# Optimization experiments

Hardware: AMD Instinct MI355X
Metric: run time of the kernel (lower is better)

## Reference

```python
import jax, jax.numpy as jnp
import numpy as np

B, N, C, NH = 32, 1024, 768, 12
KS = 3
KK = KS * KS
HD = C // NH
SCALE = HD ** -0.5
PMD = 2 * C   # patch_mix_dims = int(2 * dim)
CMD = 2 * C   # channel_mix_dims = int(2 * dim)


def _ln(x, g, b, eps):
    m = jnp.mean(x, axis=-1, keepdims=True)
    v = jnp.var(x, axis=-1, keepdims=True)
    return (x - m) * jax.lax.rsqrt(v + eps) * g + b


def setup_inputs() -> dict:
    key = jax.random.key(0)
    ks = jax.random.split(key, 12)
    w = lambda k, shape: jax.random.normal(k, shape, jnp.float32) * 0.02
    return dict(
        x=jax.random.normal(ks[0], (B, N, C), jnp.float32),
        H=32, W=32,
        kernel=w(ks[1], (KK, C)),                 # nn.Parameter, std 0.02
        ln_g=jnp.ones((C,), jnp.float32), ln_b=jnp.zeros((C,), jnp.float32),
        kv_w=w(ks[2], (C, 2 * C)),                # kv Linear, no bias (qkv_bias=False)
        proj_w=w(ks[3], (C, C)), proj_b=jnp.zeros((C,), jnp.float32),
        projq_w=w(ks[4], (C, C)),                 # proj_q, no bias
        n1_g=jnp.ones((C,), jnp.float32), n1_b=jnp.zeros((C,), jnp.float32),
        n2_g=jnp.ones((C,), jnp.float32), n2_b=jnp.zeros((C,), jnp.float32),
        pm1_w=w(ks[5], (KK, PMD)), pm1_b=jnp.zeros((PMD,), jnp.float32),
        pm2_w=w(ks[6], (PMD, KK)), pm2_b=jnp.zeros((KK,), jnp.float32),
        cm1_w=w(ks[7], (C, CMD)), cm1_b=jnp.zeros((CMD,), jnp.float32),
        cm2_w=w(ks[8], (CMD, C)), cm2_b=jnp.zeros((C,), jnp.float32),
    )


def reference(x, H, W, kernel, ln_g, ln_b, kv_w, proj_w, proj_b, projq_w,
              n1_g, n1_b, n2_g, n2_b, pm1_w, pm1_b, pm2_w, pm2_b,
              cm1_w, cm1_b, cm2_w, cm2_b):
    Bv, Nv, Cv = x.shape
    # w: expand learned 3x3 token kernel to batch -> [B, 9, C]
    w0 = jnp.broadcast_to(kernel, (Bv, KK, Cv))
    # queries from LN(kernel): [B, nh, 9, hd]
    wm = _ln(w0, ln_g, ln_b, 1e-6).reshape(Bv, KK, NH, HD).transpose(0, 2, 1, 3)
    # keys/values from x: [B, nh, N, hd]
    kv = (x @ kv_w).reshape(Bv, Nv, 2, NH, HD)
    k = kv[:, :, 0].transpose(0, 2, 1, 3)
    v = kv[:, :, 1].transpose(0, 2, 1, 3)
    attn = jax.nn.softmax(jnp.einsum('bhqd,bhkd->bhqk', wm, k) * SCALE, axis=-1)
    ca = jnp.einsum('bhqk,bhkd->bhqd', attn, v).transpose(0, 2, 1, 3).reshape(Bv, KK, Cv)
    ca = ca @ proj_w + proj_b
    w1 = w0 + ca                                  # [B, 9, C]
    # MLPMixer layer (drop_path = 0 -> identity)
    t = _ln(w1, n1_g, n1_b, 1e-5).transpose(0, 2, 1)              # [B, C, 9]
    t = jax.nn.gelu(t @ pm1_w + pm1_b, approximate=False) @ pm2_w + pm2_b
    w1 = w1 + t.transpose(0, 2, 1)
    t = _ln(w1, n2_g, n2_b, 1e-5)
    w1 = w1 + (jax.nn.gelu(t @ cm1_w + cm1_b, approximate=False) @ cm2_w + cm2_b)
    # dynamic per-(batch,channel) 3x3 depthwise conv
    filt = w1.transpose(0, 2, 1).reshape(Bv * Cv, 1, KS, KS)       # [B*C, 1, 3, 3]
    xq = (x @ projq_w).transpose(0, 2, 1).reshape(1, Bv * Cv, H, W)
    y = jax.lax.conv_general_dilated(
        xq, filt, window_strides=(1, 1), padding=((1, 1), (1, 1)),
        feature_group_count=Bv * Cv,
        dimension_numbers=('NCHW', 'OIHW', 'NCHW'))
    return y.reshape(Bv, Cv, H * W).transpose(0, 2, 1)             # [B, N, C]
```

## Files before the change

kernel.cpp:

```cpp
#include <hip/hip_runtime.h>
#include <hip/hip_bf16.h>
#include <cstdint>
#include <cstddef>

typedef __attribute__((ext_vector_type(8))) short bf16x8;
typedef __attribute__((ext_vector_type(4))) float f32x4;

#define BB 32
#define NN 1024
#define CC 768
#define NHH 12
#define HDD 64
#define KKK 9
#define MM (BB * NN)
#define KN2 1664
#define PMDD 1536
#define CMDD 1536
#define BK 64

#define XBF_BLOCKS 12288
#define WT_BLOCKS 1152
#define WT2_BLOCKS 2880
#define SW_BLOCKS 128

__device__ __forceinline__ float bfbits2f(short s) {
  union { uint32_t u; float f; } cv;
  cv.u = ((uint32_t)(uint16_t)s) << 16;
  return cv.f;
}
__device__ __forceinline__ short f2bf(float f) {
  union { float f; uint32_t u; } cv;
  cv.f = f;
  uint32_t u = cv.u;
  uint32_t r = (u + 0x7fffu + ((u >> 16) & 1u)) >> 16;
  return (short)r;
}
__device__ __forceinline__ float gelu_f(float x) {
  return 0.5f * x * (1.0f + erff(x * 0.7071067811865476f));
}

typedef const __attribute__((address_space(1))) uint32_t* gp1_t;
typedef __attribute__((address_space(3))) uint32_t* lp3_t;
__device__ __forceinline__ void gload16(const short* g, const short* l) {
  __builtin_amdgcn_global_load_lds((gp1_t)(uintptr_t)(const void*)g,
                                   (lp3_t)(uint32_t)(uintptr_t)(const void*)l,
                                   16, 0, 0);
}

__global__ __launch_bounds__(256) void prep_kernel(
    const float* __restrict__ x, short* __restrict__ xb,
    const float* __restrict__ kv_w, const float* __restrict__ projq_w,
    short* __restrict__ Wt,
    const float* __restrict__ proj_w, const float* __restrict__ cm1_w,
    const float* __restrict__ cm2_w,
    short* __restrict__ WpT, short* __restrict__ Wc1T, short* __restrict__ Wc2T,
    const float* __restrict__ kern, const float* __restrict__ ln_g,
    const float* __restrict__ ln_b)
{
  __shared__ float smem[1056];
  const int bx = blockIdx.x;
  const int tid = threadIdx.x;
  if (bx < XBF_BLOCKS) {
    const int i = (bx * 256 + tid) * 8;
    f32x4 a = *(const f32x4*)&x[i];
    f32x4 b = *(const f32x4*)&x[i + 4];
    bf16x8 o;
#pragma unroll
    for (int e = 0; e < 4; e++) { o[e] = f2bf(a[e]); o[e + 4] = f2bf(b[e]); }
    *(bf16x8*)&xb[i] = o;
    return;
  }
  if (bx < XBF_BLOCKS + WT_BLOCKS) {
    int b2 = bx - XBF_BLOCKS;
    int j0 = (b2 % 48) * 32;
    int c0 = (b2 / 48) * 32;
    const float* src; int ldj, jj;
    if (j0 < 768) { src = kv_w; ldj = 1536; jj = 768 + j0; }
    else          { src = projq_w; ldj = 768; jj = j0 - 768; }
    const int tx = tid & 31, ty = tid >> 5;
#pragma unroll
    for (int r = 0; r < 4; r++) {
      int cl = ty + r * 8;
      smem[cl * 33 + tx] = src[(size_t)(c0 + cl) * ldj + jj + tx];
    }
    __syncthreads();
#pragma unroll
    for (int r = 0; r < 4; r++) {
      int jl = ty + r * 8;
      Wt[(size_t)(j0 + jl) * CC + c0 + tx] = f2bf(smem[tx * 33 + jl]);
    }
    return;
  }
  if (bx < XBF_BLOCKS + WT_BLOCKS + WT2_BLOCKS) {
    int b2 = bx - XBF_BLOCKS - WT_BLOCKS;
    const float* src; short* dst; int ldj, ldc, j0, c0;
    if (b2 < 576)        { src = proj_w; dst = WpT;  ldj = 768;  ldc = 768;
                           j0 = (b2 % 24) * 32; c0 = (b2 / 24) * 32; }
    else if (b2 < 1728)  { b2 -= 576; src = cm1_w; dst = Wc1T; ldj = 1536; ldc = 768;
                           j0 = (b2 % 48) * 32; c0 = (b2 / 48) * 32; }
    else                 { b2 -= 1728; src = cm2_w; dst = Wc2T; ldj = 768; ldc = 1536;
                           j0 = (b2 % 24) * 32; c0 = (b2 / 24) * 32; }
    const int tx = tid & 31, ty = tid >> 5;
#pragma unroll
    for (int r = 0; r < 4; r++) {
      int cl = ty + r * 8;
      smem[cl * 33 + tx] = src[(size_t)(c0 + cl) * ldj + j0 + tx];
    }
    __syncthreads();
#pragma unroll
    for (int r = 0; r < 4; r++) {
      int jl = ty + r * 8;
      dst[(size_t)(j0 + jl) * ldc + c0 + tx] = f2bf(smem[tx * 33 + jl]);
    }
    return;
  }
  {
    const int s = bx - (XBF_BLOCKS + WT_BLOCKS + WT2_BLOCKS);
    if (s >= 108) {
      const size_t r = (size_t)(1536 + s) * CC;
      Wt[r + tid] = 0; Wt[r + tid + 256] = 0; Wt[r + tid + 512] = 0;
      return;
    }
    const int h = s / 9, q = s % 9;
    float* red = smem;
    const size_t base = (size_t)q * CC;
    float x0 = kern[base + tid];
    float x1 = kern[base + tid + 256];
    float x2 = kern[base + tid + 512];
    red[tid] = x0 + x1 + x2;
    __syncthreads();
    for (int st = 128; st > 0; st >>= 1) { if (tid < st) red[tid] += red[tid + st]; __syncthreads(); }
    float mean = red[0] * (1.0f / 768.0f);
    __syncthreads();
    float d0 = x0 - mean, d1 = x1 - mean, d2 = x2 - mean;
    red[tid] = d0 * d0 + d1 * d1 + d2 * d2;
    __syncthreads();
    for (int st = 128; st > 0; st >>= 1) { if (tid < st) red[tid] += red[tid + st]; __syncthreads(); }
    float rstd = rsqrtf(red[0] * (1.0f / 768.0f) + 1e-6f);
    __syncthreads();
    smem[tid]       = d0 * rstd * ln_g[tid]       + ln_b[tid];
    smem[tid + 256] = d1 * rstd * ln_g[tid + 256] + ln_b[tid + 256];
    smem[tid + 512] = d2 * rstd * ln_g[tid + 512] + ln_b[tid + 512];
    __syncthreads();
#pragma unroll
    for (int k = 0; k < 3; k++) {
      const int cc = tid + k * 256;
      const float* kw = &kv_w[(size_t)cc * 1536 + h * HDD];
      float acc = 0.f;
#pragma unroll
      for (int dd = 0; dd < HDD; dd++) acc += smem[h * HDD + dd] * kw[dd];
      Wt[(size_t)(1536 + s) * CC + cc] = f2bf(acc * 0.125f);
    }
  }
}

__global__ __launch_bounds__(256) void gemm_bt_kernel(
    const short* __restrict__ A,
    const short* __restrict__ Bt,
    short* __restrict__ C)
{
  __shared__ short As[2][128 * BK];
  __shared__ short Bs[2][128 * BK];
  const int tid = threadIdx.x;
  const int wave = tid >> 6, lane = tid & 63;
  const int lid = blockIdx.x;
  const int wid = (lid & 7) * 416 + (lid >> 3);
  const int bn = (wid % 13) * 128;
  const int bm = (wid / 13) * 128;
  const int wmo = (wave >> 1) * 64;
  const int wno = (wave & 1) * 64;
  const int lrow = lane & 15;
  const int kgrp = lane >> 4;
  const int sr = tid >> 3;
  const int ss = tid & 7;
  const int slotG = ss ^ (sr & 7);
  const short* gA = A + (size_t)(bm + sr) * CC + slotG * 8;
  const short* gB = Bt + (size_t)(bn + sr) * CC + slotG * 8;
  const int rs0 = kgrp ^ (lrow & 7);
  const int rs1 = (4 + kgrp) ^ (lrow & 7);
  f32x4 acc[4][4];
#pragma unroll
  for (int i = 0; i < 4; i++)
#pragma unroll
    for (int j = 0; j < 4; j++) acc[i][j] = (f32x4){0.f, 0.f, 0.f, 0.f};

#define STAGE(bb, k0)                                                          \
  {                                                                            \
    _Pragma("unroll")                                                          \
    for (int i = 0; i < 4; i++) {                                              \
      gload16(gA + (size_t)(i * 32) * CC + (k0),                               \
              &As[bb][(i * 32 + sr) * BK + ss * 8]);                           \
      gload16(gB + (size_t)(i * 32) * CC + (k0),                               \
              &Bs[bb][(i * 32 + sr) * BK + ss * 8]);                           \
    }                                                                          \
  }

  STAGE(0, 0);
  for (int t = 0; t < 12; ++t) {
    const int cur = t & 1;
    if (t < 11) STAGE(cur ^ 1, (t + 1) * BK);
    __builtin_amdgcn_sched_barrier(0);
    if (t < 11) asm volatile("s_waitcnt vmcnt(8)" ::: "memory");
    else        asm volatile("s_waitcnt vmcnt(0)" ::: "memory");
    __builtin_amdgcn_s_barrier();
    __builtin_amdgcn_sched_barrier(0);
#pragma unroll
    for (int kh = 0; kh < 2; kh++) {
      const int rs = kh ? rs1 : rs0;
      bf16x8 af[4], bfr[4];
#pragma unroll
      for (int i = 0; i < 4; i++)
        af[i] = *(const bf16x8*)&As[cur][(wmo + i * 16 + lrow) * BK + rs * 8];
#pragma unroll
      for (int j = 0; j < 4; j++)
        bfr[j] = *(const bf16x8*)&Bs[cur][(wno + j * 16 + lrow) * BK + rs * 8];
      __builtin_amdgcn_s_setprio(1);
#pragma unroll
      for (int i = 0; i < 4; i++)
#pragma unroll
        for (int j = 0; j < 4; j++)
          acc[i][j] = __builtin_amdgcn_mfma_f32_16x16x32_bf16(af[i], bfr[j], acc[i][j], 0, 0, 0);
      __builtin_amdgcn_s_setprio(0);
    }
    __builtin_amdgcn_sched_barrier(0);
    __builtin_amdgcn_s_barrier();
  }
#undef STAGE
#pragma unroll
  for (int i = 0; i < 4; i++)
#pragma unroll
    for (int j = 0; j < 4; j++)
#pragma unroll
      for (int r = 0; r < 4; r++) {
        const int row = bm + wmo + i * 16 + kgrp * 4 + r;
        const int col = bn + wno + j * 16 + lrow;
        C[(size_t)row * KN2 + col] = f2bf(acc[i][j][r]);
      }
}

template <int EP>
__global__ __launch_bounds__(256) void mfma96_kernel(
    const short* __restrict__ A,
    const short* __restrict__ Bt,
    int K, int ldn,
    const float* __restrict__ bias,
    const float* __restrict__ kern,
    float* __restrict__ Cf,
    short* __restrict__ Cb)
{
  __shared__ short As[2][96 * BK];
  __shared__ short Bs[2][128 * BK];
  const int tid = threadIdx.x;
  const int wave = tid >> 6, lane = tid & 63;
  const int bm = blockIdx.x * 96;
  const int bn = blockIdx.y * 128;
  const int wmo = (wave >> 1) * 48;
  const int wno = (wave & 1) * 64;
  const int lrow = lane & 15;
  const int kgrp = lane >> 4;
  const int sr = tid >> 3;
  const int ss = tid & 7;
  const int rs0 = kgrp ^ (lrow & 7);
  const int rs1 = (4 + kgrp) ^ (lrow & 7);
  f32x4 acc[3][4];
#pragma unroll
  for (int i = 0; i < 3; i++)
#pragma unroll
    for (int j = 0; j < 4; j++) acc[i][j] = (f32x4){0.f, 0.f, 0.f, 0.f};

#define STAGEM(bb, k0)                                                         \
  {                                                                            \
    _Pragma("unroll")                                                          \
    for (int i = 0; i < 3; i++) {                                              \
      const int r = i * 32 + sr;                                               \
      const int sg = ss ^ (r & 7);                                             \
      gload16(A + (size_t)(bm + r) * K + (k0) + sg * 8,                        \
              &As[bb][r * BK + ss * 8]);                                       \
    }                                                                          \
    _Pragma("unroll")                                                          \
    for (int i = 0; i < 4; i++) {                                              \
      const int r = i * 32 + sr;                                               \
      const int sg = ss ^ (r & 7);                                             \
      gload16(Bt + (size_t)(bn + r) * K + (k0) + sg * 8,                       \
              &Bs[bb][r * BK + ss * 8]);                                       \
    }                                                                          \
  }

  const int nt = K / BK;
  STAGEM(0, 0);
  for (int t = 0; t < nt; ++t) {
    const int cur = t & 1;
    if (t < nt - 1) STAGEM(cur ^ 1, (t + 1) * BK);
    __builtin_amdgcn_sched_barrier(0);
    if (t < nt - 1) asm volatile("s_waitcnt vmcnt(7)" ::: "memory");
    else            asm volatile("s_waitcnt vmcnt(0)" ::: "memory");
    __builtin_amdgcn_s_barrier();
    __builtin_amdgcn_sched_barrier(0);
#pragma unroll
    for (int kh = 0; kh < 2; kh++) {
      const int rs = kh ? rs1 : rs0;
      bf16x8 af[3], bfr[4];
#pragma unroll
      for (int m = 0; m < 3; m++)
        af[m] = *(const bf16x8*)&As[cur][(wmo + m * 16 + lrow) * BK + rs * 8];
#pragma unroll
      for (int n = 0; n < 4; n++)
        bfr[n] = *(const bf16x8*)&Bs[cur][(wno + n * 16 + lrow) * BK + rs * 8];
#pragma unroll
      for (int m = 0; m < 3; m++)
#pragma unroll
        for (int n = 0; n < 4; n++)
          acc[m][n] = __builtin_amdgcn_mfma_f32_16x16x32_bf16(af[m], bfr[n], acc[m][n], 0, 0, 0);
    }
    __builtin_amdgcn_sched_barrier(0);
    __builtin_amdgcn_s_barrier();
  }
#undef STAGEM
#pragma unroll
  for (int m = 0; m < 3; m++)
#pragma unroll
    for (int n = 0; n < 4; n++)
#pragma unroll
      for (int r = 0; r < 4; r++) {
        const int row = bm + wmo + m * 16 + kgrp * 4 + r;
        const int col = bn + wno + n * 16 + lrow;
        float v = acc[m][n][r] + bias[col];
        if (EP == 0) Cf[(size_t)row * ldn + col] = v + kern[(row % KKK) * ldn + col];
        if (EP == 1) Cb[(size_t)row * ldn + col] = f2bf(gelu_f(v));
        if (EP == 2) Cf[(size_t)row * ldn + col] += v;
      }
}

__global__ __launch_bounds__(256) void row_ln_bf_kernel(
    const float* __restrict__ in, short* __restrict__ out,
    const float* __restrict__ g, const float* __restrict__ bb, float eps)
{
  const int row = blockIdx.x;
  const int tid = threadIdx.x;
  __shared__ float red[256];
  const size_t base = (size_t)row * CC;
  float x0 = in[base + tid];
  float x1 = in[base + tid + 256];
  float x2 = in[base + tid + 512];
  red[tid] = x0 + x1 + x2;
  __syncthreads();
  for (int st = 128; st > 0; st >>= 1) { if (tid < st) red[tid] += red[tid + st]; __syncthreads(); }
  float mean = red[0] * (1.0f / 768.0f);
  __syncthreads();
  float d0 = x0 - mean, d1 = x1 - mean, d2 = x2 - mean;
  red[tid] = d0 * d0 + d1 * d1 + d2 * d2;
  __syncthreads();
  for (int st = 128; st > 0; st >>= 1) { if (tid < st) red[tid] += red[tid + st]; __syncthreads(); }
  float rstd = rsqrtf(red[0] * (1.0f / 768.0f) + eps);
  out[base + tid]       = f2bf(d0 * rstd * g[tid]       + bb[tid]);
  out[base + tid + 256] = f2bf(d1 * rstd * g[tid + 256] + bb[tid + 256]);
  out[base + tid + 512] = f2bf(d2 * rstd * g[tid + 512] + bb[tid + 512]);
}

__global__ __launch_bounds__(256) void attn_kernel(
    const short* __restrict__ big,
    short* __restrict__ ca)
{
  const int b = blockIdx.x;
  const int h = blockIdx.y;
  const int tid = threadIdx.x;
  const int wave = tid >> 6, lane = tid & 63;
  __shared__ float sc[KKK][NN];
  __shared__ float part[4][KKK][HDD];
#pragma unroll
  for (int nn = 0; nn < 4; nn++) {
    const int n = tid + nn * 256;
    const short* sp = &big[(size_t)(b * NN + n) * KN2 + 1536 + h * 9];
#pragma unroll
    for (int q = 0; q < KKK; q++) sc[q][n] = bfbits2f(sp[q]);
  }
  __syncthreads();
  for (int q = wave; q < KKK; q += 4) {
    float m = -1e30f;
#pragma unroll
    for (int i = 0; i < 16; i++) m = fmaxf(m, sc[q][lane + i * 64]);
#pragma unroll
    for (int off = 32; off > 0; off >>= 1) m = fmaxf(m, __shfl_xor(m, off));
    float s = 0.f;
#pragma unroll
    for (int i = 0; i < 16; i++) {
      float e = expf(sc[q][lane + i * 64] - m);
      sc[q][lane + i * 64] = e;
      s += e;
    }
#pragma unroll
    for (int off = 32; off > 0; off >>= 1) s += __shfl_xor(s, off);
    float inv = 1.0f / s;
#pragma unroll
    for (int i = 0; i < 16; i++) sc[q][lane + i * 64] *= inv;
  }
  __syncthreads();
  const int d = tid & 63, prt = tid >> 6;
  float po[KKK];
#pragma unroll
  for (int q = 0; q < KKK; q++) po[q] = 0.f;
  const short* vbase = &big[(size_t)(b * NN) * KN2 + h * HDD + d];
  for (int n0 = prt * 256; n0 < prt * 256 + 256; n0 += 4) {
    f32x4 p[KKK];
#pragma unroll
    for (int q = 0; q < KKK; q++) p[q] = *(const f32x4*)&sc[q][n0];
#pragma unroll
    for (int j = 0; j < 4; j++) {
      float vf = bfbits2f(vbase[(size_t)(n0 + j) * KN2]);
#pragma unroll
      for (int q = 0; q < KKK; q++) po[q] += p[q][j] * vf;
    }
  }
#pragma unroll
  for (int q = 0; q < KKK; q++) part[prt][q][d] = po[q];
  __syncthreads();
  for (int i = tid; i < KKK * HDD; i += 256) {
    int q = i >> 6, dd = i & 63;
    ca[(size_t)(b * KKK + q) * CC + h * HDD + dd] =
        f2bf(part[0][q][dd] + part[1][q][dd] + part[2][q][dd] + part[3][q][dd]);
  }
}

__global__ __launch_bounds__(256) void token_mix_kernel(
    const short* __restrict__ ln1,
    const float* __restrict__ pm1_w,
    const float* __restrict__ pm1_b,
    const float* __restrict__ pm2_w,
    float* __restrict__ part)
{
  const int tid = threadIdx.x;
  const int c = blockIdx.x * 256 + tid;
  const int b = blockIdx.y;
  const int jc = blockIdx.z;
  float u[KKK], o[KKK];
#pragma unroll
  for (int q = 0; q < KKK; q++) {
    u[q] = bfbits2f(ln1[(size_t)(b * KKK + q) * CC + c]);
    o[q] = 0.f;
  }
  const int j0 = jc * (PMDD / 8);
  for (int j = j0; j < j0 + PMDD / 8; j++) {
    float hs = pm1_b[j];
#pragma unroll
    for (int q = 0; q < KKK; q++) hs += u[q] * pm1_w[q * PMDD + j];
    float gv = gelu_f(hs);
    const float* p2 = &pm2_w[(size_t)j * KKK];
#pragma unroll
    for (int q = 0; q < KKK; q++) o[q] += gv * p2[q];
  }
  float* pp = &part[(size_t)((jc * BB + b) * KKK) * CC + c];
#pragma unroll
  for (int q = 0; q < KKK; q++) pp[(size_t)q * CC] = o[q];
}

__global__ __launch_bounds__(256) void token_reduce_ln_kernel(
    const float* __restrict__ part,
    const float* __restrict__ pm2_b,
    const float* __restrict__ g, const float* __restrict__ bb,
    float* __restrict__ w1,
    short* __restrict__ lnb)
{
  const int row = blockIdx.x;
  const int q = row % KKK;
  const int tid = threadIdx.x;
  __shared__ float red[256];
  const size_t base = (size_t)row * CC;
  float v[3];
#pragma unroll
  for (int j = 0; j < 3; j++) {
    const int c = tid + j * 256;
    float s = 0.f;
#pragma unroll
    for (int gg = 0; gg < 8; gg++)
      s += part[(size_t)gg * BB * KKK * CC + base + c];
    v[j] = w1[base + c] + s + pm2_b[q];
    w1[base + c] = v[j];
  }
  red[tid] = v[0] + v[1] + v[2];
  __syncthreads();
  for (int st = 128; st > 0; st >>= 1) { if (tid < st) red[tid] += red[tid + st]; __syncthreads(); }
  float mean = red[0] * (1.0f / 768.0f);
  __syncthreads();
  float d0 = v[0] - mean, d1 = v[1] - mean, d2 = v[2] - mean;
  red[tid] = d0 * d0 + d1 * d1 + d2 * d2;
  __syncthreads();
  for (int st = 128; st > 0; st >>= 1) { if (tid < st) red[tid] += red[tid + st]; __syncthreads(); }
  float rstd = rsqrtf(red[0] * (1.0f / 768.0f) + 1e-5f);
  lnb[base + tid]       = f2bf(d0 * rstd * g[tid]       + bb[tid]);
  lnb[base + tid + 256] = f2bf(d1 * rstd * g[tid + 256] + bb[tid + 256]);
  lnb[base + tid + 512] = f2bf(d2 * rstd * g[tid + 512] + bb[tid + 512]);
}

__global__ __launch_bounds__(256) void conv_lds_kernel(
    const short* __restrict__ big,
    const float* __restrict__ w1,
    float* __restrict__ out)
{
  __shared__ short rows[3][32][132];
  const int c0 = blockIdx.x * 128;
  const int b = blockIdx.y;
  const int y0 = blockIdx.z * 8;
  const int tid = threadIdx.x;
  const int xl = tid >> 3, cg = tid & 7;
  const int cl = tid & 127, xh = tid >> 7;
  float f[KKK];
#pragma unroll
  for (int q = 0; q < KKK; q++) f[q] = w1[(size_t)(b * KKK + q) * CC + c0 + cl];

#define LOAD_ROW(yy, slot)                                                     \
  {                                                                            \
    short* dst = &rows[slot][xl][cg * 16];                                     \
    if ((yy) >= 0 && (yy) < 32) {                                              \
      const short* src =                                                       \
          &big[(size_t)(b * NN + (yy) * 32 + xl) * KN2 + CC + c0 + cg * 16];   \
      *(bf16x8*)dst = *(const bf16x8*)src;                                     \
      *(bf16x8*)(dst + 8) = *(const bf16x8*)(src + 8);                         \
    } else {                                                                   \
      bf16x8 z = {0, 0, 0, 0, 0, 0, 0, 0};                                     \
      *(bf16x8*)dst = z;                                                       \
      *(bf16x8*)(dst + 8) = z;                                                 \
    }                                                                          \
  }

  int sPrev = 0, sCur = 1, sNext = 2;
  LOAD_ROW(y0 - 1, 0);
  LOAD_ROW(y0, 1);
  for (int y = y0; y < y0 + 8; ++y) {
    LOAD_ROW(y + 1, sNext);
    __syncthreads();
    const int xb = xh * 16;
    float v0[3], v1[3];
#pragma unroll
    for (int ky = 0; ky < 3; ky++) {
      const int s = (ky == 0) ? sPrev : (ky == 1 ? sCur : sNext);
      v1[ky] = bfbits2f(rows[s][xb][cl]);
      v0[ky] = (xb == 0) ? 0.f : bfbits2f(rows[s][xb - 1][cl]);
    }
    float* op = &out[(size_t)(b * NN + y * 32 + xb) * CC + c0 + cl];
#pragma unroll
    for (int i = 0; i < 16; i++) {
      const int x = xb + i;
      float v2[3];
#pragma unroll
      for (int ky = 0; ky < 3; ky++) {
        const int s = (ky == 0) ? sPrev : (ky == 1 ? sCur : sNext);
        v2[ky] = (x + 1 < 32) ? bfbits2f(rows[s][x + 1][cl]) : 0.f;
      }
      float acc = 0.f;
#pragma unroll
      for (int ky = 0; ky < 3; ky++)
        acc += f[ky * 3] * v0[ky] + f[ky * 3 + 1] * v1[ky] + f[ky * 3 + 2] * v2[ky];
      op[(size_t)i * CC] = acc;
#pragma unroll
      for (int ky = 0; ky < 3; ky++) { v0[ky] = v1[ky]; v1[ky] = v2[ky]; }
    }
    __syncthreads();
    const int t = sPrev; sPrev = sCur; sCur = sNext; sNext = t;
  }
#undef LOAD_ROW
}

extern "C" void kernel_launch(void* const* d_in, const int* in_sizes, int n_in,
                              void* d_out, int out_size, void* d_ws, size_t ws_size,
                              hipStream_t stream) {
  (void)in_sizes; (void)n_in; (void)out_size; (void)ws_size;
  const float* x       = (const float*)d_in[0];
  const float* kern    = (const float*)d_in[3];
  const float* ln_g    = (const float*)d_in[4];
  const float* ln_b    = (const float*)d_in[5];
  const float* kv_w    = (const float*)d_in[6];
  const float* proj_w  = (const float*)d_in[7];
  const float* proj_b  = (const float*)d_in[8];
  const float* projq_w = (const float*)d_in[9];
  const float* n1_g    = (const float*)d_in[10];
  const float* n1_b    = (const float*)d_in[11];
  const float* n2_g    = (const float*)d_in[12];
  const float* n2_b    = (const float*)d_in[13];
  const float* pm1_w   = (const float*)d_in[14];
  const float* pm1_b   = (const float*)d_in[15];
  const float* pm2_w   = (const float*)d_in[16];
  const float* pm2_b   = (const float*)d_in[17];
  const float* cm1_w   = (const float*)d_in[18];
  const float* cm1_b   = (const float*)d_in[19];
  const float* cm2_w   = (const float*)d_in[20];
  const float* cm2_b   = (const float*)d_in[21];
  float* out = (float*)d_out;

  uint8_t* ws = (uint8_t*)d_ws;
  short* Wt   = (short*)(ws);
  short* h1   = (short*)(ws);
  short* big  = (short*)(ws + 3538944);
  short* cab  = (short*)(ws + 154561536);
  float* w1   = (float*)(ws + 155446272);
  short* ln1b = (short*)(ws + 156331008);
  short* ln2b = (short*)(ws + 156773376);

  short* xb    = (short*)d_out;
  float* tpart = (float*)d_out;
  short* WpT   = (short*)((uint8_t*)d_out + 62914560);
  short* Wc1T  = (short*)((uint8_t*)d_out + 64094208);
  short* Wc2T  = (short*)((uint8_t*)d_out + 66453504);

  prep_kernel<<<dim3(XBF_BLOCKS + WT_BLOCKS + WT2_BLOCKS + SW_BLOCKS), 256, 0, stream>>>(
      x, xb, kv_w, projq_w, Wt, proj_w, cm1_w, cm2_w, WpT, Wc1T, Wc2T,
      kern, ln_g, ln_b);
  gemm_bt_kernel<<<dim3((MM / 128) * (KN2 / 128)), 256, 0, stream>>>(xb, Wt, big);
  attn_kernel<<<dim3(BB, NHH), 256, 0, stream>>>(big, cab);
  mfma96_kernel<0><<<dim3(3, 6), 256, 0, stream>>>(cab, WpT, CC, CC,
                                                   proj_b, kern, w1, nullptr);
  row_ln_bf_kernel<<<dim3(BB * KKK), 256, 0, stream>>>(w1, ln1b, n1_g, n1_b, 1e-5f);
  token_mix_kernel<<<dim3(3, 32, 8), 256, 0, stream>>>(ln1b, pm1_w, pm1_b, pm2_w, tpart);
  token_reduce_ln_kernel<<<dim3(BB * KKK), 256, 0, stream>>>(tpart, pm2_b,
                                                             n2_g, n2_b, w1, ln2b);
  mfma96_kernel<1><<<dim3(3, 12), 256, 0, stream>>>(ln2b, Wc1T, CC, CMDD,
                                                    cm1_b, nullptr, nullptr, h1);
  mfma96_kernel<2><<<dim3(3, 6), 256, 0, stream>>>(h1, Wc2T, CMDD, CC,
                                                   cm2_b, nullptr, w1, nullptr);
  conv_lds_kernel<<<dim3(6, 32, 4), 256, 0, stream>>>(big, w1, out);
}
```

Before: 350.4 us.

## Enlarge KV/Q projection GEMM tile to 256x256 with 512-thread blocks

The main x-projection GEMM moves from 128x128 tiles with 4 waves to 256x256 tiles with 8 waves, each wave computing a 128x64 sub-tile. The output width is padded from 1664 to 1792 so it divides by 256, and the weight-prep block count is doubled to match. The goal is more operand reuse per LDS load and less global traffic per FLOP. In exchange it does wasted work on the padded columns, uses far more LDS and registers per block, which limits occupancy to one block, and leaves a ragged final wave of blocks.

```diff
diff --git a/kernel.cpp b/kernel.cpp
--- a/kernel.cpp
+++ b/kernel.cpp
@@ -13,7 +13,7 @@
 #define HDD 64
 #define KKK 9
 #define MM (BB * NN)
-#define KN2 1664
+#define KN2 1792
 #define PMDD 1536
 #define CMDD 1536
 #define BK 64
@@ -21,7 +21,7 @@
 #define XBF_BLOCKS 12288
 #define WT_BLOCKS 1152
 #define WT2_BLOCKS 2880
-#define SW_BLOCKS 128
+#define SW_BLOCKS 256
 
 __device__ __forceinline__ float bfbits2f(short s) {
   union { uint32_t u; float f; } cv;
@@ -154,21 +154,21 @@
   }
 }
 
-__global__ __launch_bounds__(256) void gemm_bt_kernel(
+__global__ __launch_bounds__(512, 1) void gemm_bt_kernel(
     const short* __restrict__ A,
     const short* __restrict__ Bt,
     short* __restrict__ C)
 {
-  __shared__ short As[2][128 * BK];
-  __shared__ short Bs[2][128 * BK];
+  __shared__ short As[2][256 * BK];
+  __shared__ short Bs[2][256 * BK];
   const int tid = threadIdx.x;
   const int wave = tid >> 6, lane = tid & 63;
   const int lid = blockIdx.x;
-  const int wid = (lid & 7) * 416 + (lid >> 3);
-  const int bn = (wid % 13) * 128;
-  const int bm = (wid / 13) * 128;
-  const int wmo = (wave >> 1) * 64;
-  const int wno = (wave & 1) * 64;
+  const int wid = (lid & 7) * 112 + (lid >> 3);
+  const int bn = (wid % 7) * 256;
+  const int bm = (wid / 7) * 256;
+  const int wm = wave >> 2;
+  const int wn = wave & 3;
   const int lrow = lane & 15;
   const int kgrp = lane >> 4;
   const int sr = tid >> 3;
@@ -176,11 +176,9 @@
   const int slotG = ss ^ (sr & 7);
   const short* gA = A + (size_t)(bm + sr) * CC + slotG * 8;
   const short* gB = Bt + (size_t)(bn + sr) * CC + slotG * 8;
-  const int rs0 = kgrp ^ (lrow & 7);
-  const int rs1 = (4 + kgrp) ^ (lrow & 7);
-  f32x4 acc[4][4];
-#pragma unroll
-  for (int i = 0; i < 4; i++)
+  f32x4 acc[8][4];
+#pragma unroll
+  for (int i = 0; i < 8; i++)
 #pragma unroll
     for (int j = 0; j < 4; j++) acc[i][j] = (f32x4){0.f, 0.f, 0.f, 0.f};
 
@@ -188,10 +186,10 @@
   {                                                                            \
     _Pragma("unroll")                                                          \
     for (int i = 0; i < 4; i++) {                                              \
-      gload16(gA + (size_t)(i * 32) * CC + (k0),                               \
-              &As[bb][(i * 32 + sr) * BK + ss * 8]);                           \
-      gload16(gB + (size_t)(i * 32) * CC + (k0),                               \
-              &Bs[bb][(i * 32 + sr) * BK + ss * 8]);                           \
+      gload16(gA + (size_t)(i * 64) * CC + (k0),                               \
+              &As[bb][(i * 64 + sr) * BK + ss * 8]);                           \
+      gload16(gB + (size_t)(i * 64) * CC + (k0),                               \
+              &Bs[bb][(i * 64 + sr) * BK + ss * 8]);                           \
     }                                                                          \
   }
 
@@ -206,20 +204,20 @@
     __builtin_amdgcn_sched_barrier(0);
 #pragma unroll
     for (int kh = 0; kh < 2; kh++) {
-      const int rs = kh ? rs1 : rs0;
-      bf16x8 af[4], bfr[4];
-#pragma unroll
-      for (int i = 0; i < 4; i++)
-        af[i] = *(const bf16x8*)&As[cur][(wmo + i * 16 + lrow) * BK + rs * 8];
-#pragma unroll
-      for (int j = 0; j < 4; j++)
-        bfr[j] = *(const bf16x8*)&Bs[cur][(wno + j * 16 + lrow) * BK + rs * 8];
+      const int rs = ((kh * 4 + kgrp) ^ (lrow & 7));
+      bf16x8 af[8], bfr[4];
+#pragma unroll
+      for (int m = 0; m < 8; m++)
+        af[m] = *(const bf16x8*)&As[cur][(wm * 128 + m * 16 + lrow) * BK + rs * 8];
+#pragma unroll
+      for (int n = 0; n < 4; n++)
+        bfr[n] = *(const bf16x8*)&Bs[cur][(wn * 64 + n * 16 + lrow) * BK + rs * 8];
       __builtin_amdgcn_s_setprio(1);
 #pragma unroll
-      for (int i = 0; i < 4; i++)
-#pragma unroll
-        for (int j = 0; j < 4; j++)
-          acc[i][j] = __builtin_amdgcn_mfma_f32_16x16x32_bf16(af[i], bfr[j], acc[i][j], 0, 0, 0);
+      for (int m = 0; m < 8; m++)
+#pragma unroll
+        for (int n = 0; n < 4; n++)
+          acc[m][n] = __builtin_amdgcn_mfma_f32_16x16x32_bf16(af[m], bfr[n], acc[m][n], 0, 0, 0);
       __builtin_amdgcn_s_setprio(0);
     }
     __builtin_amdgcn_sched_barrier(0);
@@ -227,14 +225,14 @@
   }
 #undef STAGE
 #pragma unroll
-  for (int i = 0; i < 4; i++)
-#pragma unroll
-    for (int j = 0; j < 4; j++)
+  for (int m = 0; m < 8; m++)
+#pragma unroll
+    for (int n = 0; n < 4; n++)
 #pragma unroll
       for (int r = 0; r < 4; r++) {
-        const int row = bm + wmo + i * 16 + kgrp * 4 + r;
-        const int col = bn + wno + j * 16 + lrow;
-        C[(size_t)row * KN2 + col] = f2bf(acc[i][j][r]);
+        const int row = bm + wm * 128 + m * 16 + kgrp * 4 + r;
+        const int col = bn + wn * 64 + n * 16 + lrow;
+        C[(size_t)row * KN2 + col] = f2bf(acc[m][n][r]);
       }
 }
 
@@ -604,7 +602,7 @@
   prep_kernel<<<dim3(XBF_BLOCKS + WT_BLOCKS + WT2_BLOCKS + SW_BLOCKS), 256, 0, stream>>>(
       x, xb, kv_w, projq_w, Wt, proj_w, cm1_w, cm2_w, WpT, Wc1T, Wc2T,
       kern, ln_g, ln_b);
-  gemm_bt_kernel<<<dim3((MM / 128) * (KN2 / 128)), 256, 0, stream>>>(xb, Wt, big);
+  gemm_bt_kernel<<<dim3((MM / 256) * (KN2 / 256)), 512, 0, stream>>>(xb, Wt, big);
   attn_kernel<<<dim3(BB, NHH), 256, 0, stream>>>(big, cab);
   mfma96_kernel<0><<<dim3(3, 6), 256, 0, stream>>>(cab, WpT, CC, CC,
                                                    proj_b, kern, w1, nullptr);
```

Measured after the change: 367.4 us. 4.9% more time.
